# Kernel tuning notes

Hardware: AMD Instinct MI355X
Metric: run time of the kernel (lower is better)

## Reference

```python
import jax, jax.numpy as jnp
import numpy as np

D = 128  # input_dim

def setup_inputs() -> dict:
    key = jax.random.key(0)
    ks = jax.random.split(key, 9)
    B, Lq, Lkv = 4, 4096, 4096
    s = 1.0 / np.sqrt(D)
    return {
        "x1": jax.random.normal(ks[0], (B, Lq, D), dtype=jnp.float32),
        "x2": jax.random.normal(ks[1], (B, Lkv, D), dtype=jnp.float32),
        "x3": jax.random.normal(ks[2], (B, Lkv, D), dtype=jnp.float32),
        "Wq": jax.random.normal(ks[3], (D, D), dtype=jnp.float32) * s,
        "bq": jax.random.normal(ks[4], (D,), dtype=jnp.float32) * s,
        "Wk": jax.random.normal(ks[5], (D, D), dtype=jnp.float32) * s,
        "bk": jax.random.normal(ks[6], (D,), dtype=jnp.float32) * s,
        "Wv": jax.random.normal(ks[7], (D, D), dtype=jnp.float32) * s,
        "bv": jax.random.normal(ks[8], (D,), dtype=jnp.float32) * s,
    }

def reference(x1, x2, x3, Wq, bq, Wk, bk, Wv, bv):
    # torch Linear: y = x @ W.T + b
    q = jnp.einsum('bld,ed->ble', x1, Wq) + bq  # [B,Lq,D]
    k = jnp.einsum('bld,ed->ble', x2, Wk) + bk  # [B,Lkv,D]
    v = jnp.einsum('bld,ed->ble', x3, Wv) + bv  # [B,Lkv,D]
    scores = jnp.einsum('bqd,bkd->bqk', q, k) / jnp.sqrt(jnp.float32(x1.shape[-1]))
    attn = jax.nn.softmax(scores, axis=2)
    return jnp.einsum('bqk,bkd->bqd', attn, v)
```

## Files before the change

### kernel.cpp

```cpp
#include <hip/hip_runtime.h>
#include <hip/hip_bf16.h>

typedef __attribute__((ext_vector_type(8))) short short8;
typedef __attribute__((ext_vector_type(4))) float v4f;

__device__ __forceinline__ unsigned short f2bf(float f) {
    union { float f; unsigned u; } c; c.f = f;
    unsigned r = c.u + 0x7FFFu + ((c.u >> 16) & 1u);
    return (unsigned short)(r >> 16);
}
__device__ __forceinline__ unsigned pack2(float a, float b) {
    return (unsigned)f2bf(a) | ((unsigned)f2bf(b) << 16);
}
__device__ __forceinline__ float bf2f(unsigned short h) {
    union { unsigned u; float f; } c; c.u = ((unsigned)h) << 16;
    return c.f;
}

__device__ __forceinline__ void g2l16(const unsigned short* g, unsigned short* l) {
    __builtin_amdgcn_global_load_lds(
        (const __attribute__((address_space(1))) unsigned int*)g,
        (__attribute__((address_space(3))) unsigned int*)l,
        16, 0, 0);
}

__global__ __launch_bounds__(512) void proj_kernel(
    const float* __restrict__ x1, const float* __restrict__ x2, const float* __restrict__ x3,
    const float* __restrict__ Wq, const float* __restrict__ bq,
    const float* __restrict__ Wk, const float* __restrict__ bk,
    const float* __restrict__ Wv, const float* __restrict__ bv,
    unsigned short* __restrict__ qb, unsigned short* __restrict__ kb,
    unsigned short* __restrict__ vb, float qscale)
{
    __shared__ __attribute__((aligned(16))) unsigned short Xs[16384];
    __shared__ __attribute__((aligned(16))) unsigned short Ws[16384];

    int tid = threadIdx.x;
    int wave = tid >> 6, lane = tid & 63;
    int lmod = lane & 15, ldiv = lane >> 4;
    int p = blockIdx.x % 3;
    int row0 = (blockIdx.x / 3) * 128;

    const float* X = p == 0 ? x1 : p == 1 ? x2 : x3;
    const float* W = p == 0 ? Wq : p == 1 ? Wk : Wv;
    const float* bias = p == 0 ? bq : p == 1 ? bk : bv;
    float scale = p == 0 ? qscale : 1.0f;

#pragma unroll
    for (int i = 0; i < 8; i++) {
        int c = tid + i * 512;
        int row = c >> 5, d0 = (c & 31) * 4;
        v4f f = *(const v4f*)(X + (size_t)(row0 + row) * 128 + d0);
        int off = ((row >> 4) * 16 + (d0 >> 5) * 4 + ((d0 >> 3) & 3)) * 128 + (row & 15) * 8 + (d0 & 7);
        *(uint2*)&Xs[off] = make_uint2(pack2(f[0], f[1]), pack2(f[2], f[3]));
        v4f g = *(const v4f*)(W + (size_t)row * 128 + d0);
        *(uint2*)&Ws[off] = make_uint2(pack2(g[0], g[1]), pack2(g[2], g[3]));
    }
    __syncthreads();

    short8 af[4];
#pragma unroll
    for (int kc = 0; kc < 4; kc++)
        af[kc] = *(const short8*)&Xs[wave * 2048 + (kc * 4 + ldiv) * 128 + lmod * 8];

#pragma unroll
    for (int ct = 0; ct < 8; ct++) {
        v4f acc = {0.f, 0.f, 0.f, 0.f};
#pragma unroll
        for (int kc = 0; kc < 4; kc++) {
            short8 bf = *(const short8*)&Ws[ct * 2048 + (kc * 4 + ldiv) * 128 + lmod * 8];
            acc = __builtin_amdgcn_mfma_f32_16x16x32_bf16(af[kc], bf, acc, 0, 0, 0);
        }
        int e = ct * 16 + lmod;
        float bv_ = bias[e];
#pragma unroll
        for (int r = 0; r < 4; r++) {
            int orow = row0 + wave * 16 + ldiv * 4 + r;
            unsigned short h = f2bf((acc[r] + bv_) * scale);
            if (p == 0) {
                qb[(size_t)orow * 128 + e] = h;
            } else if (p == 1) {
                int b = orow >> 12, key = orow & 4095, kk = key & 31;
                kb[b * 524288 + (key >> 5) * 4096 + (kk & 1) * 2048
                   + ((e >> 5) * 4 + ((e >> 3) & 3)) * 128 + (kk >> 1) * 8 + (e & 7)] = h;
            } else {
                int b = orow >> 12, key = orow & 4095;
                vb[b * 524288 + (key >> 5) * 4096
                   + ((e >> 4) * 4 + ((key >> 3) & 3)) * 128 + (e & 15) * 8 + (key & 7)] = h;
            }
        }
    }
}

__global__ __launch_bounds__(256, 2) void attn_kernel(
    const unsigned short* __restrict__ Qb,
    const unsigned short* __restrict__ Kb,
    const unsigned short* __restrict__ Vb,
    unsigned short* __restrict__ Opart,
    float* __restrict__ Lbuf)
{
    __shared__ __attribute__((aligned(16))) unsigned short Kt[2][4096];
    __shared__ __attribute__((aligned(16))) unsigned short Vt[2][4096];
    __shared__ __attribute__((aligned(16))) unsigned short Ps[4][1280];

    int tid = threadIdx.x;
    int wave = tid >> 6, lane = tid & 63;
    int lmod = lane & 15, ldiv = lane >> 4;
    int split = blockIdx.x & 3;
    int qidx = blockIdx.x >> 2;
    int b = qidx >> 5;
    int q0 = (qidx & 31) * 128 + wave * 32;

    short8 qfrag[2][4];
#pragma unroll
    for (int set = 0; set < 2; set++) {
        const unsigned short* qptr = Qb + (size_t)(b * 4096 + q0 + set * 16 + lmod) * 128;
#pragma unroll
        for (int kc = 0; kc < 4; kc++)
            qfrag[set][kc] = *(const short8*)(qptr + kc * 32 + ldiv * 8);
    }

    v4f oacc[2][8];
#pragma unroll
    for (int set = 0; set < 2; set++)
#pragma unroll
        for (int dt = 0; dt < 8; dt++) oacc[set][dt] = (v4f){0.f, 0.f, 0.f, 0.f};
    float lsum[2][4] = {{0.f, 0.f, 0.f, 0.f}, {0.f, 0.f, 0.f, 0.f}};

    const unsigned short* kbase = Kb + b * 524288 + split * 131072;
    const unsigned short* vbase = Vb + b * 524288 + split * 131072;

#pragma unroll
    for (int i = 0; i < 2; i++) {
        g2l16(kbase + wave * 1024 + i * 512 + lane * 8, &Kt[0][wave * 1024 + i * 512]);
        g2l16(vbase + wave * 1024 + i * 512 + lane * 8, &Vt[0][wave * 1024 + i * 512]);
    }
    __syncthreads();

    for (int t = 0; t < 32; t++) {
        int cur = t & 1;
        if (t < 31) {
            const unsigned short* kg = kbase + (t + 1) * 4096;
            const unsigned short* vg = vbase + (t + 1) * 4096;
#pragma unroll
            for (int i = 0; i < 2; i++) {
                g2l16(kg + wave * 1024 + i * 512 + lane * 8, &Kt[cur ^ 1][wave * 1024 + i * 512]);
                g2l16(vg + wave * 1024 + i * 512 + lane * 8, &Vt[cur ^ 1][wave * 1024 + i * 512]);
            }
        }

        v4f sacc[2][2];
#pragma unroll
        for (int set = 0; set < 2; set++)
#pragma unroll
            for (int s = 0; s < 2; s++) sacc[set][s] = (v4f){0.f, 0.f, 0.f, 0.f};
#pragma unroll
        for (int kc = 0; kc < 4; kc++) {
            short8 kf0 = *(const short8*)&Kt[cur][(kc * 4 + ldiv) * 128 + lmod * 8];
            short8 kf1 = *(const short8*)&Kt[cur][2048 + (kc * 4 + ldiv) * 128 + lmod * 8];
            sacc[0][0] = __builtin_amdgcn_mfma_f32_16x16x32_bf16(qfrag[0][kc], kf0, sacc[0][0], 0, 0, 0);
            sacc[0][1] = __builtin_amdgcn_mfma_f32_16x16x32_bf16(qfrag[0][kc], kf1, sacc[0][1], 0, 0, 0);
            sacc[1][0] = __builtin_amdgcn_mfma_f32_16x16x32_bf16(qfrag[1][kc], kf0, sacc[1][0], 0, 0, 0);
            sacc[1][1] = __builtin_amdgcn_mfma_f32_16x16x32_bf16(qfrag[1][kc], kf1, sacc[1][1], 0, 0, 0);
        }

#pragma unroll
        for (int set = 0; set < 2; set++)
#pragma unroll
            for (int r = 0; r < 4; r++) {
                float p0 = __builtin_amdgcn_exp2f(sacc[set][0][r]);
                float p1 = __builtin_amdgcn_exp2f(sacc[set][1][r]);
                lsum[set][r] += p0 + p1;
                *(unsigned*)&Ps[wave][(set * 16 + 4 * ldiv + r) * 40 + lmod * 2] = pack2(p0, p1);
            }
        asm volatile("s_waitcnt lgkmcnt(0)" ::: "memory");

        short8 pf0 = *(const short8*)&Ps[wave][lmod * 40 + ldiv * 8];
        short8 pf1 = *(const short8*)&Ps[wave][(16 + lmod) * 40 + ldiv * 8];
#pragma unroll
        for (int dt = 0; dt < 8; dt++) {
            short8 vf = *(const short8*)&Vt[cur][(dt * 4 + ldiv) * 128 + lmod * 8];
            oacc[0][dt] = __builtin_amdgcn_mfma_f32_16x16x32_bf16(pf0, vf, oacc[0][dt], 0, 0, 0);
            oacc[1][dt] = __builtin_amdgcn_mfma_f32_16x16x32_bf16(pf1, vf, oacc[1][dt], 0, 0, 0);
        }
        __syncthreads();
    }

#pragma unroll
    for (int set = 0; set < 2; set++)
#pragma unroll
        for (int r = 0; r < 4; r++) {
            float lv = lsum[set][r];
            lv += __shfl_xor(lv, 1);
            lv += __shfl_xor(lv, 2);
            lv += __shfl_xor(lv, 4);
            lv += __shfl_xor(lv, 8);
            int gq = b * 4096 + q0 + set * 16 + 4 * ldiv + r;
            if (lmod == 0) Lbuf[split * 16384 + gq] = lv;
            unsigned short* obase = Opart + (size_t)(split * 16384 + gq) * 128;
#pragma unroll
            for (int dt = 0; dt < 8; dt++)
                obase[dt * 16 + lmod] = f2bf(oacc[set][dt][r]);
        }
}

__global__ __launch_bounds__(256) void merge_kernel(
    const unsigned short* __restrict__ Opart,
    const float* __restrict__ Lbuf,
    float* __restrict__ Out)
{
    int t = blockIdx.x * 256 + threadIdx.x;
#pragma unroll
    for (int it = 0; it < 4; it++) {
        int base = (t + it * 65536) * 8;
        int q = base >> 7;
        float inv = 1.0f / (Lbuf[q] + Lbuf[16384 + q] + Lbuf[32768 + q] + Lbuf[49152 + q]);
        float acc[8] = {0.f, 0.f, 0.f, 0.f, 0.f, 0.f, 0.f, 0.f};
#pragma unroll
        for (int s = 0; s < 4; s++) {
            short8 o = *(const short8*)(Opart + (size_t)s * 2097152 + base);
#pragma unroll
            for (int j = 0; j < 8; j++) acc[j] += bf2f((unsigned short)o[j]);
        }
        v4f lo = {acc[0] * inv, acc[1] * inv, acc[2] * inv, acc[3] * inv};
        v4f hi = {acc[4] * inv, acc[5] * inv, acc[6] * inv, acc[7] * inv};
        *(v4f*)(Out + base) = lo;
        *(v4f*)(Out + base + 4) = hi;
    }
}

extern "C" void kernel_launch(void* const* d_in, const int* in_sizes, int n_in,
                              void* d_out, int out_size, void* d_ws, size_t ws_size,
                              hipStream_t stream) {
    const float* x1 = (const float*)d_in[0];
    const float* x2 = (const float*)d_in[1];
    const float* x3 = (const float*)d_in[2];
    const float* Wq = (const float*)d_in[3];
    const float* bq = (const float*)d_in[4];
    const float* Wk = (const float*)d_in[5];
    const float* bk = (const float*)d_in[6];
    const float* Wv = (const float*)d_in[7];
    const float* bv = (const float*)d_in[8];
    float* out = (float*)d_out;

    unsigned short* qb = (unsigned short*)d_ws;
    unsigned short* kb = qb + (size_t)2097152;
    unsigned short* vb = kb + (size_t)2097152;
    unsigned short* op = vb + (size_t)2097152;
    float* lb = (float*)(op + (size_t)8388608);

    const float qscale = 1.4426950408889634f / 11.313708498984761f;

    proj_kernel<<<384, 512, 0, stream>>>(x1, x2, x3, Wq, bq, Wk, bk, Wv, bv,
                                         qb, kb, vb, qscale);
    attn_kernel<<<512, 256, 0, stream>>>(qb, kb, vb, op, lb);
    merge_kernel<<<256, 256, 0, stream>>>(op, lb, out);
}
```

Baseline: 140.8 us.

## Stage projection output in LDS, load K/V directly to registers, split KV eight ways

The projection kernel now writes its bf16 results into shared memory in the target layout, then copies them out with coalesced 16-byte stores instead of scattered 2-byte stores. The attention kernel drops the double-buffered LDS staging and barriers for K/V and loads fragments straight from global memory into registers. It also doubles the KV split to 8, with 1024 blocks and occupancy hint 4, so more work runs in parallel. In exchange, the merge kernel has twice as much partial output to read and reduce, and K/V reads now rely on cache hits instead of LDS reuse.

```diff
diff --git a/kernel.cpp b/kernel.cpp
--- a/kernel.cpp
+++ b/kernel.cpp
@@ -3,6 +3,7 @@
 
 typedef __attribute__((ext_vector_type(8))) short short8;
 typedef __attribute__((ext_vector_type(4))) float v4f;
+typedef __attribute__((ext_vector_type(4))) unsigned int uint4v;
 
 __device__ __forceinline__ unsigned short f2bf(float f) {
     union { float f; unsigned u; } c; c.f = f;
@@ -15,13 +16,6 @@
 __device__ __forceinline__ float bf2f(unsigned short h) {
     union { unsigned u; float f; } c; c.u = ((unsigned)h) << 16;
     return c.f;
-}
-
-__device__ __forceinline__ void g2l16(const unsigned short* g, unsigned short* l) {
-    __builtin_amdgcn_global_load_lds(
-        (const __attribute__((address_space(1))) unsigned int*)g,
-        (__attribute__((address_space(3))) unsigned int*)l,
-        16, 0, 0);
 }
 
 __global__ __launch_bounds__(512) void proj_kernel(
@@ -32,8 +26,10 @@
     unsigned short* __restrict__ qb, unsigned short* __restrict__ kb,
     unsigned short* __restrict__ vb, float qscale)
 {
-    __shared__ __attribute__((aligned(16))) unsigned short Xs[16384];
-    __shared__ __attribute__((aligned(16))) unsigned short Ws[16384];
+    __shared__ __attribute__((aligned(16))) unsigned short Smem[32768];
+    unsigned short* Xs = Smem;
+    unsigned short* Ws = Smem + 16384;
+    unsigned short* Os = Smem;
 
     int tid = threadIdx.x;
     int wave = tid >> 6, lane = tid & 63;
@@ -62,6 +58,7 @@
 #pragma unroll
     for (int kc = 0; kc < 4; kc++)
         af[kc] = *(const short8*)&Xs[wave * 2048 + (kc * 4 + ldiv) * 128 + lmod * 8];
+    __syncthreads();
 
 #pragma unroll
     for (int ct = 0; ct < 8; ct++) {
@@ -75,39 +72,54 @@
         float bv_ = bias[e];
 #pragma unroll
         for (int r = 0; r < 4; r++) {
-            int orow = row0 + wave * 16 + ldiv * 4 + r;
+            int lrow = wave * 16 + ldiv * 4 + r;
             unsigned short h = f2bf((acc[r] + bv_) * scale);
+            int off;
             if (p == 0) {
-                qb[(size_t)orow * 128 + e] = h;
+                off = lrow * 128 + e;
             } else if (p == 1) {
-                int b = orow >> 12, key = orow & 4095, kk = key & 31;
-                kb[b * 524288 + (key >> 5) * 4096 + (kk & 1) * 2048
-                   + ((e >> 5) * 4 + ((e >> 3) & 3)) * 128 + (kk >> 1) * 8 + (e & 7)] = h;
+                int kk = lrow & 31, c = lrow >> 5;
+                off = c * 4096 + (kk & 1) * 2048
+                    + ((e >> 5) * 4 + ((e >> 3) & 3)) * 128 + (kk >> 1) * 8 + (e & 7);
             } else {
-                int b = orow >> 12, key = orow & 4095;
-                vb[b * 524288 + (key >> 5) * 4096
-                   + ((e >> 4) * 4 + ((key >> 3) & 3)) * 128 + (e & 15) * 8 + (key & 7)] = h;
+                int kk = lrow & 31, c = lrow >> 5;
+                off = c * 4096 + ((e >> 4) * 4 + ((kk >> 3) & 3)) * 128
+                    + (e & 15) * 8 + (kk & 7);
             }
-        }
-    }
-}
-
-__global__ __launch_bounds__(256, 2) void attn_kernel(
+            Os[off] = h;
+        }
+    }
+    __syncthreads();
+
+    unsigned short* dst;
+    size_t gbase;
+    if (p == 0) { dst = qb; gbase = (size_t)row0 * 128; }
+    else {
+        int b = row0 >> 12, key0 = row0 & 4095;
+        gbase = (size_t)b * 524288 + (key0 >> 5) * 4096;
+        dst = (p == 1) ? kb : vb;
+    }
+#pragma unroll
+    for (int i = 0; i < 4; i++) {
+        int c = (tid + i * 512) * 8;
+        *(uint4v*)(dst + gbase + c) = *(const uint4v*)&Os[c];
+    }
+}
+
+__global__ __launch_bounds__(256, 4) void attn_kernel(
     const unsigned short* __restrict__ Qb,
     const unsigned short* __restrict__ Kb,
     const unsigned short* __restrict__ Vb,
     unsigned short* __restrict__ Opart,
     float* __restrict__ Lbuf)
 {
-    __shared__ __attribute__((aligned(16))) unsigned short Kt[2][4096];
-    __shared__ __attribute__((aligned(16))) unsigned short Vt[2][4096];
-    __shared__ __attribute__((aligned(16))) unsigned short Ps[4][1280];
+    __shared__ __attribute__((aligned(16))) unsigned short PsB[4][1280];
 
     int tid = threadIdx.x;
     int wave = tid >> 6, lane = tid & 63;
     int lmod = lane & 15, ldiv = lane >> 4;
-    int split = blockIdx.x & 3;
-    int qidx = blockIdx.x >> 2;
+    int split = blockIdx.x & 7;
+    int qidx = blockIdx.x >> 3;
     int b = qidx >> 5;
     int q0 = (qidx & 31) * 128 + wave * 32;
 
@@ -127,26 +139,19 @@
         for (int dt = 0; dt < 8; dt++) oacc[set][dt] = (v4f){0.f, 0.f, 0.f, 0.f};
     float lsum[2][4] = {{0.f, 0.f, 0.f, 0.f}, {0.f, 0.f, 0.f, 0.f}};
 
-    const unsigned short* kbase = Kb + b * 524288 + split * 131072;
-    const unsigned short* vbase = Vb + b * 524288 + split * 131072;
-
-#pragma unroll
-    for (int i = 0; i < 2; i++) {
-        g2l16(kbase + wave * 1024 + i * 512 + lane * 8, &Kt[0][wave * 1024 + i * 512]);
-        g2l16(vbase + wave * 1024 + i * 512 + lane * 8, &Vt[0][wave * 1024 + i * 512]);
-    }
-    __syncthreads();
-
-    for (int t = 0; t < 32; t++) {
-        int cur = t & 1;
-        if (t < 31) {
-            const unsigned short* kg = kbase + (t + 1) * 4096;
-            const unsigned short* vg = vbase + (t + 1) * 4096;
-#pragma unroll
-            for (int i = 0; i < 2; i++) {
-                g2l16(kg + wave * 1024 + i * 512 + lane * 8, &Kt[cur ^ 1][wave * 1024 + i * 512]);
-                g2l16(vg + wave * 1024 + i * 512 + lane * 8, &Vt[cur ^ 1][wave * 1024 + i * 512]);
-            }
+    const unsigned short* kbase = Kb + (size_t)b * 524288 + split * 65536;
+    const unsigned short* vbase = Vb + (size_t)b * 524288 + split * 65536;
+    unsigned short* Ps = PsB[wave];
+
+    for (int t = 0; t < 16; t++) {
+        const unsigned short* Kt = kbase + t * 4096;
+        const unsigned short* Vt = vbase + t * 4096;
+
+        short8 kf0[4], kf1[4];
+#pragma unroll
+        for (int kc = 0; kc < 4; kc++) {
+            kf0[kc] = *(const short8*)(Kt + (kc * 4 + ldiv) * 128 + lmod * 8);
+            kf1[kc] = *(const short8*)(Kt + 2048 + (kc * 4 + ldiv) * 128 + lmod * 8);
         }
 
         v4f sacc[2][2];
@@ -156,13 +161,16 @@
             for (int s = 0; s < 2; s++) sacc[set][s] = (v4f){0.f, 0.f, 0.f, 0.f};
 #pragma unroll
         for (int kc = 0; kc < 4; kc++) {
-            short8 kf0 = *(const short8*)&Kt[cur][(kc * 4 + ldiv) * 128 + lmod * 8];
-            short8 kf1 = *(const short8*)&Kt[cur][2048 + (kc * 4 + ldiv) * 128 + lmod * 8];
-            sacc[0][0] = __builtin_amdgcn_mfma_f32_16x16x32_bf16(qfrag[0][kc], kf0, sacc[0][0], 0, 0, 0);
-            sacc[0][1] = __builtin_amdgcn_mfma_f32_16x16x32_bf16(qfrag[0][kc], kf1, sacc[0][1], 0, 0, 0);
-            sacc[1][0] = __builtin_amdgcn_mfma_f32_16x16x32_bf16(qfrag[1][kc], kf0, sacc[1][0], 0, 0, 0);
-            sacc[1][1] = __builtin_amdgcn_mfma_f32_16x16x32_bf16(qfrag[1][kc], kf1, sacc[1][1], 0, 0, 0);
-        }
+            sacc[0][0] = __builtin_amdgcn_mfma_f32_16x16x32_bf16(qfrag[0][kc], kf0[kc], sacc[0][0], 0, 0, 0);
+            sacc[0][1] = __builtin_amdgcn_mfma_f32_16x16x32_bf16(qfrag[0][kc], kf1[kc], sacc[0][1], 0, 0, 0);
+            sacc[1][0] = __builtin_amdgcn_mfma_f32_16x16x32_bf16(qfrag[1][kc], kf0[kc], sacc[1][0], 0, 0, 0);
+            sacc[1][1] = __builtin_amdgcn_mfma_f32_16x16x32_bf16(qfrag[1][kc], kf1[kc], sacc[1][1], 0, 0, 0);
+        }
+
+        short8 vf[8];
+#pragma unroll
+        for (int dt = 0; dt < 8; dt++)
+            vf[dt] = *(const short8*)(Vt + (dt * 4 + ldiv) * 128 + lmod * 8);
 
 #pragma unroll
         for (int set = 0; set < 2; set++)
@@ -171,19 +179,17 @@
                 float p0 = __builtin_amdgcn_exp2f(sacc[set][0][r]);
                 float p1 = __builtin_amdgcn_exp2f(sacc[set][1][r]);
                 lsum[set][r] += p0 + p1;
-                *(unsigned*)&Ps[wave][(set * 16 + 4 * ldiv + r) * 40 + lmod * 2] = pack2(p0, p1);
+                *(unsigned*)&Ps[(set * 16 + 4 * ldiv + r) * 40 + lmod * 2] = pack2(p0, p1);
             }
         asm volatile("s_waitcnt lgkmcnt(0)" ::: "memory");
 
-        short8 pf0 = *(const short8*)&Ps[wave][lmod * 40 + ldiv * 8];
-        short8 pf1 = *(const short8*)&Ps[wave][(16 + lmod) * 40 + ldiv * 8];
+        short8 pf0 = *(const short8*)&Ps[lmod * 40 + ldiv * 8];
+        short8 pf1 = *(const short8*)&Ps[(16 + lmod) * 40 + ldiv * 8];
 #pragma unroll
         for (int dt = 0; dt < 8; dt++) {
-            short8 vf = *(const short8*)&Vt[cur][(dt * 4 + ldiv) * 128 + lmod * 8];
-            oacc[0][dt] = __builtin_amdgcn_mfma_f32_16x16x32_bf16(pf0, vf, oacc[0][dt], 0, 0, 0);
-            oacc[1][dt] = __builtin_amdgcn_mfma_f32_16x16x32_bf16(pf1, vf, oacc[1][dt], 0, 0, 0);
-        }
-        __syncthreads();
+            oacc[0][dt] = __builtin_amdgcn_mfma_f32_16x16x32_bf16(pf0, vf[dt], oacc[0][dt], 0, 0, 0);
+            oacc[1][dt] = __builtin_amdgcn_mfma_f32_16x16x32_bf16(pf1, vf[dt], oacc[1][dt], 0, 0, 0);
+        }
     }
 
 #pragma unroll
@@ -214,18 +220,19 @@
     for (int it = 0; it < 4; it++) {
         int base = (t + it * 65536) * 8;
         int q = base >> 7;
-        float inv = 1.0f / (Lbuf[q] + Lbuf[16384 + q] + Lbuf[32768 + q] + Lbuf[49152 + q]);
+        float lt = 0.f;
+#pragma unroll
+        for (int s = 0; s < 8; s++) lt += Lbuf[s * 16384 + q];
+        float inv = 1.0f / lt;
         float acc[8] = {0.f, 0.f, 0.f, 0.f, 0.f, 0.f, 0.f, 0.f};
 #pragma unroll
-        for (int s = 0; s < 4; s++) {
+        for (int s = 0; s < 8; s++) {
             short8 o = *(const short8*)(Opart + (size_t)s * 2097152 + base);
 #pragma unroll
             for (int j = 0; j < 8; j++) acc[j] += bf2f((unsigned short)o[j]);
         }
-        v4f lo = {acc[0] * inv, acc[1] * inv, acc[2] * inv, acc[3] * inv};
-        v4f hi = {acc[4] * inv, acc[5] * inv, acc[6] * inv, acc[7] * inv};
-        *(v4f*)(Out + base) = lo;
-        *(v4f*)(Out + base + 4) = hi;
+        *(v4f*)(Out + base) = (v4f){acc[0] * inv, acc[1] * inv, acc[2] * inv, acc[3] * inv};
+        *(v4f*)(Out + base + 4) = (v4f){acc[4] * inv, acc[5] * inv, acc[6] * inv, acc[7] * inv};
     }
 }
 
@@ -247,12 +254,12 @@
     unsigned short* kb = qb + (size_t)2097152;
     unsigned short* vb = kb + (size_t)2097152;
     unsigned short* op = vb + (size_t)2097152;
-    float* lb = (float*)(op + (size_t)8388608);
+    float* lb = (float*)(op + (size_t)16777216);
 
     const float qscale = 1.4426950408889634f / 11.313708498984761f;
 
     proj_kernel<<<384, 512, 0, stream>>>(x1, x2, x3, Wq, bq, Wk, bk, Wv, bv,
                                          qb, kb, vb, qscale);
-    attn_kernel<<<512, 256, 0, stream>>>(qb, kb, vb, op, lb);
+    attn_kernel<<<1024, 256, 0, stream>>>(qb, kb, vb, op, lb);
     merge_kernel<<<256, 256, 0, stream>>>(op, lb, out);
 }
```

Result: slower. 208.7 us (+48.2%).
